# Kernel tuning notes

Measured on AMD Instinct MI355X. Metric: run time of the kernel, lower is better.

The kernel has to match this reference:

```python
import jax, jax.numpy as jnp
import numpy as np

B, C_IN, C_OUT, H, W = 128, 128, 128, 40, 40
NUM_EXPERTS, TOP_K, EXPAND = 8, 2, 2
C_HID = C_IN * EXPAND


def setup_inputs() -> dict:
    key = jax.random.key(0)
    ks = jax.random.split(key, 6)
    x = jax.random.normal(ks[0], (B, C_IN, H, W), dtype=jnp.float32)
    weights = jax.random.uniform(ks[1], (B, TOP_K), dtype=jnp.float32)
    indices = jax.random.randint(ks[2], (B, TOP_K), 0, NUM_EXPERTS, dtype=jnp.int64)
    # per-expert 1x1 conv params: expand -> SiLU -> project
    W1 = jax.random.normal(ks[3], (NUM_EXPERTS, C_HID, C_IN), dtype=jnp.float32) * (1.0 / np.sqrt(C_IN))
    b1 = jnp.zeros((NUM_EXPERTS, C_HID), dtype=jnp.float32)
    W2 = jax.random.normal(ks[4], (NUM_EXPERTS, C_OUT, C_HID), dtype=jnp.float32) * (1.0 / np.sqrt(C_HID))
    b2 = jnp.zeros((NUM_EXPERTS, C_OUT), dtype=jnp.float32)
    return {"x": x, "weights": weights, "indices": indices,
            "W1": W1, "b1": b1, "W2": W2, "b2": b2}


def reference(x, weights, indices, W1, b1, W2, b2):
    # Combine top-k gate weights per (batch, expert): duplicate expert picks sum,
    # exactly matching the original's per-expert gather + weighted index_add_.
    Bn = x.shape[0]
    E = W1.shape[0]
    gate = jnp.zeros((Bn, E), dtype=x.dtype).at[jnp.arange(Bn)[:, None], indices].add(weights)  # [B, E]
    out = jnp.zeros((Bn, W2.shape[1]) + x.shape[2:], dtype=x.dtype)
    for e in range(E):  # fixed small expert loop
        h = jax.nn.silu(jnp.einsum('bchw,oc->bohw', x, W1[e]) + b1[e][None, :, None, None])
        y = jnp.einsum('bchw,oc->bohw', h, W2[e]) + b2[e][None, :, None, None]
        out = out + y * gate[:, e][:, None, None, None]
    return out
```

## Files before the change

kernel.cpp:

```cpp
#include <hip/hip_runtime.h>

#define CIN   128
#define CHID  256
#define COUT  128
#define HWPX  1600
#define TPX   32
#define XOFF  0
#define WOFF  53248

typedef __attribute__((ext_vector_type(8))) short bf16x8;
typedef __attribute__((ext_vector_type(4))) float f32x4;

__device__ __forceinline__ unsigned short f2bf(float f) {
  unsigned int u = __builtin_bit_cast(unsigned int, f);
  u += 0x7FFFu + ((u >> 16) & 1u);
  return (unsigned short)(u >> 16);
}
__device__ __forceinline__ unsigned int pack_bf2(float a, float b) {
  return (unsigned int)f2bf(a) | ((unsigned int)f2bf(b) << 16);
}
__device__ __forceinline__ unsigned int silu_gate_pk(float a, float b, float g) {
  const float ea = __builtin_amdgcn_exp2f(a * -1.442695041f);
  const float eb = __builtin_amdgcn_exp2f(b * -1.442695041f);
  const float sa = g * a * __builtin_amdgcn_rcpf(1.0f + ea);
  const float sb = g * b * __builtin_amdgcn_rcpf(1.0f + eb);
  return pack_bf2(sa, sb);
}

__global__ __launch_bounds__(256) void convert_w_kernel(
    const float* __restrict__ W1, const float* __restrict__ W2,
    unsigned short* __restrict__ W1b, unsigned short* __restrict__ W2b) {
  const int i   = blockIdx.x * 256 + threadIdx.x;
  const int j   = i & 7;
  const int p   = (i >> 3) & 511;
  const int grp = (i >> 12) & 7;
  const int e   = i >> 15;
  {
    const int r   = p >> 4;
    const int c   = ((p & 15) - r) & 15;
    const int row = r & 15, mt = r >> 4;
    const int ch  = grp * 32 + ((row >> 2) << 3) + (row & 3) + (mt << 2);
    W1b[i] = f2bf(W1[(e * CHID + ch) * CIN + c * 8 + j]);
  }
  {
    const int co = p >> 2;
    const int c  = ((p & 3) - co - (co >> 2)) & 3;
    const int ch = grp * 32 + c * 8 + j;
    W2b[i] = f2bf(W2[(e * COUT + co) * CHID + ch]);
  }
}

__device__ __forceinline__ void stage_w(const unsigned short* W1b,
                                        const unsigned short* W2b,
                                        int e, int grp, unsigned short* wb,
                                        int wave, int lane) {
  const long s = ((long)(e * 8 + grp) << 12) + wave * 1024 + lane * 8;
#pragma unroll
  for (int k2 = 0; k2 < 2; ++k2) {
    __builtin_amdgcn_global_load_lds(
        (const __attribute__((address_space(1))) unsigned int*)(W1b + s + k2 * 512),
        (__attribute__((address_space(3))) unsigned int*)(wb + wave * 1024 + k2 * 512),
        16, 0, 0);
    __builtin_amdgcn_global_load_lds(
        (const __attribute__((address_space(1))) unsigned int*)(W2b + s + k2 * 512),
        (__attribute__((address_space(3))) unsigned int*)(wb + 4096 + wave * 1024 + k2 * 512),
        16, 0, 0);
  }
}

__global__ __launch_bounds__(256, 1) void moe_kernel(
    const float* __restrict__ x, const float* __restrict__ wts,
    const int* __restrict__ idx, const unsigned short* __restrict__ W1b,
    const float* __restrict__ b1, const unsigned short* __restrict__ W2b,
    const float* __restrict__ b2, float* __restrict__ out) {
  __shared__ __align__(16) unsigned short lds[69632];

  const int tid  = threadIdx.x;
  const int wave = tid >> 6;
  const int lane = tid & 63;
  const int q    = lane >> 4;
  const int r16  = lane & 15;

  const int b    = blockIdx.x >> 2;
  const int blkp = blockIdx.x & 3;
  const int cnt  = (blkp < 2) ? 13 : 12;
  const int T0   = blkp * 12 + (blkp < 2 ? blkp : 2);
  const int ntw  = 3 + ((cnt == 13 && wave == 0) ? 1 : 0);
  const int ws   = 3 * wave + ((cnt == 13 && wave > 0) ? 1 : 0);

  const int   e0 = __builtin_amdgcn_readfirstlane(idx[b * 2 + 0]);
  const int   e1 = __builtin_amdgcn_readfirstlane(idx[b * 2 + 1]);
  const float g0 = wts[b * 2 + 0], g1 = wts[b * 2 + 1];

  stage_w(W1b, W2b, e0, 0, &lds[WOFF + 0 * 8192], wave, lane);
  stage_w(W1b, W2b, e0, 1, &lds[WOFF + 1 * 8192], wave, lane);

  {
    const int p = lane & 31, hh = lane >> 5;
    for (int lt = ws; lt < ws + ntw; ++lt) {
      const int gt = T0 + lt;
      const float* xr = x + (long)b * CIN * HWPX + gt * TPX + p;
      unsigned short* xw = &lds[XOFF + lt * 4096];
#pragma unroll
      for (int it = 0; it < 8; ++it) {
        const int cc = it * 2 + hh;
        float v[8];
#pragma unroll
        for (int jj = 0; jj < 8; ++jj) v[jj] = xr[(long)(cc * 8 + jj) * HWPX];
        union { bf16x8 w; unsigned int u[4]; } t;
#pragma unroll
        for (int d = 0; d < 4; ++d) t.u[d] = pack_bf2(v[2 * d], v[2 * d + 1]);
        const int slot = (cc + p) & 15;
        *reinterpret_cast<bf16x8*>(&xw[(p * 16 + slot) * 8]) = t.w;
      }
    }
  }

  f32x4 accO[4][8][2];
#pragma unroll
  for (int t = 0; t < 4; ++t)
#pragma unroll
    for (int mt = 0; mt < 8; ++mt)
#pragma unroll
      for (int nt = 0; nt < 2; ++nt) accO[t][mt][nt] = (f32x4){0.f, 0.f, 0.f, 0.f};

  for (int gs = 0; gs < 16; ++gs) {
    const int   sl  = gs >> 3;
    const int   grp = gs & 7;
    const int   e   = sl ? e1 : e0;
    const float g   = sl ? g1 : g0;
    unsigned short* wb = &lds[WOFF + (gs & 1) * 8192];

    asm volatile("s_waitcnt vmcnt(4)" ::: "memory");
    __builtin_amdgcn_sched_barrier(0);
    __builtin_amdgcn_s_barrier();

    bf16x8 w1f[8];
#pragma unroll
    for (int ks = 0; ks < 4; ++ks) {
      const int slotw = (ks * 4 + q + r16) & 15;
      w1f[ks * 2 + 0] = *reinterpret_cast<const bf16x8*>(&wb[(r16 * 16 + slotw) * 8]);
      w1f[ks * 2 + 1] = *reinterpret_cast<const bf16x8*>(&wb[((r16 + 16) * 16 + slotw) * 8]);
    }
    bf16x8 w2f[8];
#pragma unroll
    for (int mt = 0; mt < 8; ++mt) {
      const int co = mt * 16 + r16;
      w2f[mt] = *reinterpret_cast<const bf16x8*>(
          &wb[4096 + (co * 4 + ((q + co + (co >> 2)) & 3)) * 8]);
    }
    const float* b1e = b1 + e * CHID + grp * 32;
    const f32x4 bA = *reinterpret_cast<const f32x4*>(&b1e[q * 8]);
    const f32x4 bB = *reinterpret_cast<const f32x4*>(&b1e[q * 8 + 4]);

#pragma unroll
    for (int t = 0; t < 4; ++t) {
      if (t < ntw) {
        const unsigned short* xw = &lds[XOFF + (ws + t) * 4096];
        f32x4 aA[2], aB[2];
#pragma unroll
        for (int nt = 0; nt < 2; ++nt) {
          aA[nt] = (f32x4){0.f, 0.f, 0.f, 0.f};
          aB[nt] = (f32x4){0.f, 0.f, 0.f, 0.f};
        }
#pragma unroll
        for (int ks = 0; ks < 4; ++ks) {
#pragma unroll
          for (int nt = 0; nt < 2; ++nt) {
            const int px = nt * 16 + r16;
            const bf16x8 xf = *reinterpret_cast<const bf16x8*>(
                &xw[(px * 16 + ((ks * 4 + q + px) & 15)) * 8]);
            aA[nt] = __builtin_amdgcn_mfma_f32_16x16x32_bf16(w1f[ks * 2 + 0], xf, aA[nt], 0, 0, 0);
            aB[nt] = __builtin_amdgcn_mfma_f32_16x16x32_bf16(w1f[ks * 2 + 1], xf, aB[nt], 0, 0, 0);
          }
        }
        union { bf16x8 v; unsigned int u[4]; } h[2];
#pragma unroll
        for (int nt = 0; nt < 2; ++nt) {
          h[nt].u[0] = silu_gate_pk(aA[nt][0] + bA[0], aA[nt][1] + bA[1], g);
          h[nt].u[1] = silu_gate_pk(aA[nt][2] + bA[2], aA[nt][3] + bA[3], g);
          h[nt].u[2] = silu_gate_pk(aB[nt][0] + bB[0], aB[nt][1] + bB[1], g);
          h[nt].u[3] = silu_gate_pk(aB[nt][2] + bB[2], aB[nt][3] + bB[3], g);
        }
#pragma unroll
        for (int mt = 0; mt < 8; ++mt)
#pragma unroll
          for (int nt = 0; nt < 2; ++nt)
            accO[t][mt][nt] = __builtin_amdgcn_mfma_f32_16x16x32_bf16(w2f[mt], h[nt].v, accO[t][mt][nt], 0, 0, 0);
      }
    }

    __builtin_amdgcn_s_barrier();
    if (gs <= 14) {
      const int gs2  = (gs + 2 <= 15) ? gs + 2 : 15;
      const int e2   = (gs2 >> 3) ? e1 : e0;
      stage_w(W1b, W2b, e2, gs2 & 7, wb, wave, lane);
    }
  }

  const float* b2e0 = b2 + e0 * COUT;
  const float* b2e1 = b2 + e1 * COUT;
  const int coR = lane >> 2;
  const int qtr = lane & 3;
#pragma unroll
  for (int t = 0; t < 4; ++t) {
    if (t < ntw) {
      float* eb = reinterpret_cast<float*>(&lds[XOFF + (ws + t) * 4096]);
      const long px0   = (long)(T0 + ws + t) * TPX;
      const long obase = (long)b * COUT * HWPX + px0;
#pragma unroll
      for (int mt = 0; mt < 8; ++mt) {
        const int coW = q * 4;
        const f32x4 bias = g0 * (*reinterpret_cast<const f32x4*>(&b2e0[mt * 16 + coW])) +
                           g1 * (*reinterpret_cast<const f32x4*>(&b2e1[mt * 16 + coW]));
#pragma unroll
        for (int nt = 0; nt < 2; ++nt) {
          const f32x4 v = accO[t][mt][nt] + bias;
#pragma unroll
          for (int rr = 0; rr < 4; ++rr)
            eb[(coW + rr) * 36 + nt * 16 + r16] = v[rr];
        }
        const long orow = obase + (long)(mt * 16 + coR) * HWPX;
#pragma unroll
        for (int k = 0; k < 2; ++k) {
          const float4 ov = *reinterpret_cast<const float4*>(
              &eb[coR * 36 + k * 16 + qtr * 4]);
          *reinterpret_cast<float4*>(&out[orow + k * 16 + qtr * 4]) = ov;
        }
      }
    }
  }
}

extern "C" void kernel_launch(void* const* d_in, const int* in_sizes, int n_in,
                              void* d_out, int out_size, void* d_ws, size_t ws_size,
                              hipStream_t stream) {
  const float* x   = (const float*)d_in[0];
  const float* wts = (const float*)d_in[1];
  const int*   idx = (const int*)d_in[2];
  const float* W1  = (const float*)d_in[3];
  const float* b1  = (const float*)d_in[4];
  const float* W2  = (const float*)d_in[5];
  const float* b2  = (const float*)d_in[6];
  float* out = (float*)d_out;

  unsigned short* W1b = (unsigned short*)d_ws;
  unsigned short* W2b = (unsigned short*)d_ws + (8 * CHID * CIN);

  convert_w_kernel<<<262144 / 256, 256, 0, stream>>>(W1, W2, W1b, W2b);
  moe_kernel<<<128 * 4, 256, 0, stream>>>(x, wts, idx, W1b, b1, W2b, b2, out);
}
```

Measured before the change: 316.4 us.

## Pre-convert x to swizzled bf16 tiles in prep kernel, async-stage into LDS

The fp32-to-bf16 conversion and swizzle of x moves into the existing weight-conversion kernel, which writes pre-laid-out bf16 tiles to workspace. The main kernel then loads them straight into LDS with async global_load_lds, overlapped with weight staging, instead of strided fp32 register loads. The epilogue is also restructured so each wave writes all its tiles to LDS scratch per mt and stores wider rows to global memory. This adds an extra global write and read of x in bf16, in exchange for shorter, latency-hidden prologue loads in the main kernel.

```diff
diff --git a/kernel.cpp b/kernel.cpp
--- a/kernel.cpp
+++ b/kernel.cpp
@@ -4,6 +4,7 @@
 #define CHID  256
 #define COUT  128
 #define HWPX  1600
+#define NT    50
 #define TPX   32
 #define XOFF  0
 #define WOFF  53248
@@ -27,10 +28,68 @@
   return pack_bf2(sa, sb);
 }
 
-__global__ __launch_bounds__(256) void convert_w_kernel(
-    const float* __restrict__ W1, const float* __restrict__ W2,
-    unsigned short* __restrict__ W1b, unsigned short* __restrict__ W2b) {
-  const int i   = blockIdx.x * 256 + threadIdx.x;
+__device__ __forceinline__ void stage_tile(const unsigned short* g,
+                                           unsigned short* l, int lane) {
+#pragma unroll
+  for (int k = 0; k < 8; ++k)
+    __builtin_amdgcn_global_load_lds(
+        (const __attribute__((address_space(1))) unsigned int*)(g + (k * 64 + lane) * 8),
+        (__attribute__((address_space(3))) unsigned int*)(l + k * 512),
+        16, 0, 0);
+}
+
+__device__ __forceinline__ void stage_w(const unsigned short* W1b,
+                                        const unsigned short* W2b,
+                                        int e, int grp, unsigned short* wb,
+                                        int wave, int lane) {
+  const long s = ((long)(e * 8 + grp) << 12) + wave * 1024 + lane * 8;
+#pragma unroll
+  for (int k2 = 0; k2 < 2; ++k2) {
+    __builtin_amdgcn_global_load_lds(
+        (const __attribute__((address_space(1))) unsigned int*)(W1b + s + k2 * 512),
+        (__attribute__((address_space(3))) unsigned int*)(wb + wave * 1024 + k2 * 512),
+        16, 0, 0);
+    __builtin_amdgcn_global_load_lds(
+        (const __attribute__((address_space(1))) unsigned int*)(W2b + s + k2 * 512),
+        (__attribute__((address_space(3))) unsigned int*)(wb + 4096 + wave * 1024 + k2 * 512),
+        16, 0, 0);
+  }
+}
+
+__global__ __launch_bounds__(256) void convert_kernel(
+    const float* __restrict__ x, const float* __restrict__ W1,
+    const float* __restrict__ W2, unsigned short* __restrict__ W1b,
+    unsigned short* __restrict__ W2b, unsigned short* __restrict__ xbf) {
+  __shared__ __align__(16) unsigned short xl[4][4096];
+  const int bid = blockIdx.x;
+  if (bid < 1664) {
+    const int wave = threadIdx.x >> 6, lane = threadIdx.x & 63;
+    const int b = bid / 13, blk = bid % 13;
+    const int tile = blk * 4 + wave;
+    if (tile >= NT) return;
+    const int p = lane & 31, hh = lane >> 5;
+    const float* xr = x + (long)b * CIN * HWPX + tile * TPX + p;
+    unsigned short* w = &xl[wave][0];
+#pragma unroll
+    for (int c = 0; c < 8; ++c) {
+      const int cc = c * 2 + hh;
+      float v[8];
+#pragma unroll
+      for (int jj = 0; jj < 8; ++jj) v[jj] = xr[(long)(cc * 8 + jj) * HWPX];
+      union { bf16x8 t; unsigned int u[4]; } t;
+#pragma unroll
+      for (int d = 0; d < 4; ++d) t.u[d] = pack_bf2(v[2 * d], v[2 * d + 1]);
+      const int slot = (cc + p) & 15;
+      *reinterpret_cast<bf16x8*>(&w[(p * 16 + slot) * 8]) = t.t;
+    }
+    uint4* dst = reinterpret_cast<uint4*>(xbf + ((long)b * NT + tile) * 4096);
+    const uint4* src = reinterpret_cast<const uint4*>(w);
+#pragma unroll
+    for (int k = 0; k < 8; ++k) dst[k * 64 + lane] = src[k * 64 + lane];
+    return;
+  }
+  const int wb2 = bid - 1664;
+  const int i   = wb2 * 256 + threadIdx.x;
   const int j   = i & 7;
   const int p   = (i >> 3) & 511;
   const int grp = (i >> 12) & 7;
@@ -50,26 +109,8 @@
   }
 }
 
-__device__ __forceinline__ void stage_w(const unsigned short* W1b,
-                                        const unsigned short* W2b,
-                                        int e, int grp, unsigned short* wb,
-                                        int wave, int lane) {
-  const long s = ((long)(e * 8 + grp) << 12) + wave * 1024 + lane * 8;
-#pragma unroll
-  for (int k2 = 0; k2 < 2; ++k2) {
-    __builtin_amdgcn_global_load_lds(
-        (const __attribute__((address_space(1))) unsigned int*)(W1b + s + k2 * 512),
-        (__attribute__((address_space(3))) unsigned int*)(wb + wave * 1024 + k2 * 512),
-        16, 0, 0);
-    __builtin_amdgcn_global_load_lds(
-        (const __attribute__((address_space(1))) unsigned int*)(W2b + s + k2 * 512),
-        (__attribute__((address_space(3))) unsigned int*)(wb + 4096 + wave * 1024 + k2 * 512),
-        16, 0, 0);
-  }
-}
-
 __global__ __launch_bounds__(256, 1) void moe_kernel(
-    const float* __restrict__ x, const float* __restrict__ wts,
+    const unsigned short* __restrict__ xbf, const float* __restrict__ wts,
     const int* __restrict__ idx, const unsigned short* __restrict__ W1b,
     const float* __restrict__ b1, const unsigned short* __restrict__ W2b,
     const float* __restrict__ b2, float* __restrict__ out) {
@@ -93,28 +134,10 @@
   const float g0 = wts[b * 2 + 0], g1 = wts[b * 2 + 1];
 
   stage_w(W1b, W2b, e0, 0, &lds[WOFF + 0 * 8192], wave, lane);
+  for (int lt = ws; lt < ws + ntw; ++lt)
+    stage_tile(xbf + ((long)b * NT + (T0 + lt)) * 4096,
+               &lds[XOFF + lt * 4096], lane);
   stage_w(W1b, W2b, e0, 1, &lds[WOFF + 1 * 8192], wave, lane);
-
-  {
-    const int p = lane & 31, hh = lane >> 5;
-    for (int lt = ws; lt < ws + ntw; ++lt) {
-      const int gt = T0 + lt;
-      const float* xr = x + (long)b * CIN * HWPX + gt * TPX + p;
-      unsigned short* xw = &lds[XOFF + lt * 4096];
-#pragma unroll
-      for (int it = 0; it < 8; ++it) {
-        const int cc = it * 2 + hh;
-        float v[8];
-#pragma unroll
-        for (int jj = 0; jj < 8; ++jj) v[jj] = xr[(long)(cc * 8 + jj) * HWPX];
-        union { bf16x8 w; unsigned int u[4]; } t;
-#pragma unroll
-        for (int d = 0; d < 4; ++d) t.u[d] = pack_bf2(v[2 * d], v[2 * d + 1]);
-        const int slot = (cc + p) & 15;
-        *reinterpret_cast<bf16x8*>(&xw[(p * 16 + slot) * 8]) = t.w;
-      }
-    }
-  }
 
   f32x4 accO[4][8][2];
 #pragma unroll
@@ -192,41 +215,45 @@
 
     __builtin_amdgcn_s_barrier();
     if (gs <= 14) {
-      const int gs2  = (gs + 2 <= 15) ? gs + 2 : 15;
-      const int e2   = (gs2 >> 3) ? e1 : e0;
+      const int gs2 = (gs + 2 <= 15) ? gs + 2 : 15;
+      const int e2  = (gs2 >> 3) ? e1 : e0;
       stage_w(W1b, W2b, e2, gs2 & 7, wb, wave, lane);
     }
   }
 
+  float* scr = reinterpret_cast<float*>(&lds[XOFF + ws * 4096]);
   const float* b2e0 = b2 + e0 * COUT;
   const float* b2e1 = b2 + e1 * COUT;
-  const int coR = lane >> 2;
-  const int qtr = lane & 3;
-#pragma unroll
-  for (int t = 0; t < 4; ++t) {
-    if (t < ntw) {
-      float* eb = reinterpret_cast<float*>(&lds[XOFF + (ws + t) * 4096]);
-      const long px0   = (long)(T0 + ws + t) * TPX;
-      const long obase = (long)b * COUT * HWPX + px0;
-#pragma unroll
-      for (int mt = 0; mt < 8; ++mt) {
-        const int coW = q * 4;
-        const f32x4 bias = g0 * (*reinterpret_cast<const f32x4*>(&b2e0[mt * 16 + coW])) +
-                           g1 * (*reinterpret_cast<const f32x4*>(&b2e1[mt * 16 + coW]));
+  const int rh   = lane >> 5;
+  const int li   = lane & 31;
+  const int tt   = li >> 3;
+  const int px4v = (li & 7) * 4;
+  const long ob  = (long)b * COUT * HWPX + (long)(T0 + ws) * TPX;
+#pragma unroll
+  for (int mt = 0; mt < 8; ++mt) {
+    const int coW = q * 4;
+    const f32x4 bias = g0 * (*reinterpret_cast<const f32x4*>(&b2e0[mt * 16 + coW])) +
+                       g1 * (*reinterpret_cast<const f32x4*>(&b2e1[mt * 16 + coW]));
+#pragma unroll
+    for (int t = 0; t < 4; ++t) {
+      if (t < ntw) {
 #pragma unroll
         for (int nt = 0; nt < 2; ++nt) {
           const f32x4 v = accO[t][mt][nt] + bias;
 #pragma unroll
           for (int rr = 0; rr < 4; ++rr)
-            eb[(coW + rr) * 36 + nt * 16 + r16] = v[rr];
-        }
-        const long orow = obase + (long)(mt * 16 + coR) * HWPX;
-#pragma unroll
-        for (int k = 0; k < 2; ++k) {
-          const float4 ov = *reinterpret_cast<const float4*>(
-              &eb[coR * 36 + k * 16 + qtr * 4]);
-          *reinterpret_cast<float4*>(&out[orow + k * 16 + qtr * 4]) = ov;
-        }
+            scr[t * 528 + (coW + rr) * 33 + nt * 16 + r16] = v[rr];
+        }
+      }
+    }
+    if (tt < ntw) {
+      const float* sb = scr + tt * 528;
+#pragma unroll
+      for (int cp = 0; cp < 8; ++cp) {
+        const int col = cp * 2 + rh;
+        const float4 v = *reinterpret_cast<const float4*>(&sb[col * 33 + px4v]);
+        *reinterpret_cast<float4*>(
+            &out[ob + (long)(mt * 16 + col) * HWPX + tt * TPX + px4v]) = v;
       }
     }
   }
@@ -245,8 +272,9 @@
   float* out = (float*)d_out;
 
   unsigned short* W1b = (unsigned short*)d_ws;
-  unsigned short* W2b = (unsigned short*)d_ws + (8 * CHID * CIN);
-
-  convert_w_kernel<<<262144 / 256, 256, 0, stream>>>(W1, W2, W1b, W2b);
-  moe_kernel<<<128 * 4, 256, 0, stream>>>(x, wts, idx, W1b, b1, W2b, b2, out);
-}
+  unsigned short* W2b = W1b + 8 * CHID * CIN;
+  unsigned short* xbf = W2b + 8 * CHID * CIN;
+
+  convert_kernel<<<1664 + 1024, 256, 0, stream>>>(x, W1, W2, W1b, W2b, xbf);
+  moe_kernel<<<128 * 4, 256, 0, stream>>>(xbf, wts, idx, W1b, b1, W2b, b2, out);
+}
```

Result: slower. 334.3 us (+5.7%).
